# Kernel optimization log

Hardware: AMD Instinct MI355X
Metric: run time of the kernel (lower is better)

## Reference

```python
import jax, jax.numpy as jnp
import numpy as np

B, S, D, H = 2, 2048, 1024, 16
HD = D // H  # head_dim = 64

def setup_inputs() -> dict:
    key = jax.random.key(0)
    ks = jax.random.split(key, 5)
    scale = 0.02
    return {
        "x":  jax.random.normal(ks[0], (B, S, D), dtype=jnp.float32),
        "Wq": jax.random.normal(ks[1], (D, D), dtype=jnp.float32) * scale,
        "Wk": jax.random.normal(ks[2], (D, D), dtype=jnp.float32) * scale,
        "Wv": jax.random.normal(ks[3], (D, D), dtype=jnp.float32) * scale,
        "Wo": jax.random.normal(ks[4], (D, D), dtype=jnp.float32) * scale,
    }

def reference(x, Wq, Wk, Wv, Wo):
    b, s, d = x.shape
    # projections (bias-free linear): [b,s,d] @ [d,d]
    q = (x @ Wq).reshape(b, s, H, HD).transpose(0, 2, 1, 3)  # [b,h,s,hd]
    k = (x @ Wk).reshape(b, s, H, HD).transpose(0, 2, 1, 3)
    v = (x @ Wv).reshape(b, s, H, HD).transpose(0, 2, 1, 3)
    scale = jnp.asarray(1.0 / np.sqrt(HD), dtype=x.dtype)
    scores = jnp.einsum('bhqd,bhkd->bhqk', q, k) * scale  # [b,h,s,s]
    causal = jnp.tril(jnp.ones((s, s), dtype=bool))
    scores = jnp.where(causal, scores, jnp.asarray(-jnp.inf, dtype=scores.dtype))
    attn = jax.nn.softmax(scores, axis=-1)
    out = jnp.einsum('bhqk,bhkd->bhqd', attn, v)  # [b,h,s,hd]
    out = out.transpose(0, 2, 1, 3).reshape(b, s, d)
    return out @ Wo
```

## Files before the change

kernel.cpp:

```cpp
#include <hip/hip_runtime.h>
#include <hip/hip_bf16.h>
#include <cstdint>

typedef __bf16 bf16;
typedef bf16 bf16x8 __attribute__((ext_vector_type(8)));
typedef bf16 bf16x4 __attribute__((ext_vector_type(4)));
typedef float f32x4 __attribute__((ext_vector_type(4)));

#define MFMA16(a, b, c) __builtin_amdgcn_mfma_f32_16x16x32_bf16(a, b, c, 0, 0, 0)

struct rawF { f32x4 a, b; };
__device__ inline rawF ldr(const float* p) {
  rawF r; r.a = *(const f32x4*)p; r.b = *(const f32x4*)(p + 4); return r;
}
__device__ inline bf16x8 ldr(const bf16* p) { return *(const bf16x8*)p; }
__device__ inline bf16x8 cv(const rawF& r) {
  bf16x8 o;
#pragma unroll
  for (int i = 0; i < 4; ++i) { o[i] = (bf16)r.a[i]; o[i + 4] = (bf16)r.b[i]; }
  return o;
}
__device__ inline bf16x8 cv(const bf16x8& r) { return r; }
__device__ inline void stC(bf16* C, size_t i, float v) { C[i] = (bf16)v; }
__device__ inline void stC(float* C, size_t i, float v) { C[i] = v; }

__device__ inline void gl16(const bf16* g, bf16* l) {
  __builtin_amdgcn_global_load_lds(
      (const __attribute__((address_space(1))) void*)g,
      (__attribute__((address_space(3))) void*)l, 16, 0, 0);
}

__device__ inline size_t tile_el(int rowg, int colg) {
  int kq = (colg >> 3) & 3;
  int s = (rowg & 15) ^ kq;
  return ((size_t)(rowg >> 7) * 32 + (colg >> 5)) * 4096 +
         (((rowg >> 6) & 1) << 11) + (((rowg >> 4) & 3) << 9) + (kq << 7) +
         (s << 3) + (colg & 7);
}

__global__ __launch_bounds__(256) void prep_wt(const float* __restrict__ W0,
                                               const float* __restrict__ W1,
                                               const float* __restrict__ W2,
                                               const float* __restrict__ W3,
                                               bf16* __restrict__ Wt, int n) {
  const float* Ws[4] = {W0, W1, W2, W3};
  const float* W = Ws[blockIdx.z];
  bf16* out = Wt + (size_t)blockIdx.z * n * n;
  __shared__ bf16 t[32][33];
  int bx = blockIdx.x * 32, by = blockIdx.y * 32;
  int tx = threadIdx.x & 31, ty = threadIdx.x >> 5;
#pragma unroll
  for (int i = 0; i < 32; i += 8)
    t[ty + i][tx] = (bf16)W[(size_t)(by + ty + i) * n + bx + tx];
  __syncthreads();
#pragma unroll
  for (int i = 0; i < 32; i += 8)
    out[(size_t)(bx + ty + i) * n + by + tx] = t[tx][ty + i];
}

__global__ __launch_bounds__(256) void prep_wt_t(const float* __restrict__ W0,
                                                 const float* __restrict__ W1,
                                                 const float* __restrict__ W2,
                                                 const float* __restrict__ W3,
                                                 bf16* __restrict__ Wt, int n) {
  const float* Ws[4] = {W0, W1, W2, W3};
  const float* W = Ws[blockIdx.z];
  bf16* out = Wt + (size_t)blockIdx.z * n * n;
  __shared__ bf16 t[32][33];
  int bx = blockIdx.x * 32, by = blockIdx.y * 32;
  int tx = threadIdx.x & 31, ty = threadIdx.x >> 5;
#pragma unroll
  for (int i = 0; i < 32; i += 8)
    t[ty + i][tx] = (bf16)W[(size_t)(by + ty + i) * n + bx + tx];
  __syncthreads();
  int tid = threadIdx.x;
  if (tid < 128) {
    int ngl = tid >> 2, kc0 = (tid & 3) * 8;
    bf16x8 o;
#pragma unroll
    for (int j = 0; j < 8; ++j) o[j] = t[kc0 + j][ngl];
    *(bf16x8*)&out[tile_el(bx + ngl, by + kc0)] = o;
  }
}

__global__ __launch_bounds__(256) void vtrans(const bf16* __restrict__ V, bf16* __restrict__ Vt) {
  constexpr int Sn = 2048, Dn = 1024;
  __shared__ bf16 L[64 * 66];
  int s0 = blockIdx.x * 64, bh = blockIdx.y;
  int b = bh >> 4, h = bh & 15;
  int t = threadIdx.x;
  int r = t >> 3, c8 = (t & 7) * 8;
#pragma unroll
  for (int half = 0; half < 2; ++half) {
    int rr = r + half * 32;
    bf16x8 v = *(const bf16x8*)&V[(size_t)(b * Sn + s0 + rr) * Dn + h * 64 + c8];
#pragma unroll
    for (int j = 0; j < 8; ++j) L[(c8 + j) * 66 + rr] = v[j];
  }
  __syncthreads();
  int hd = t >> 3;
#pragma unroll
  for (int half = 0; half < 2; ++half) {
    int hh = hd + half * 32;
    bf16x8 o;
#pragma unroll
    for (int j = 0; j < 8; ++j) o[j] = L[hh * 66 + c8 + j];
    *(bf16x8*)&Vt[(size_t)bh * 64 * Sn + (size_t)hh * Sn + s0 + c8] = o;
  }
}

template <typename TC>
__global__ __launch_bounds__(256) void gemmTh(const float* __restrict__ A,
                                              const bf16* __restrict__ B0,
                                              const bf16* __restrict__ B1,
                                              const bf16* __restrict__ B2,
                                              TC* __restrict__ C0, TC* __restrict__ C1,
                                              TC* __restrict__ C2, int nsteps, int nblk) {
  __shared__ bf16 As[2][4096];
  __shared__ bf16 Bs[2][4096];
  int tid = threadIdx.x, wave = tid >> 6, lane = tid & 63;
  int la = lane & 15, quad = lane >> 4;
  int by = blockIdx.y, sel = by / nblk, nb = by - sel * nblk;
  const bf16* Bt = sel == 0 ? B0 : (sel == 1 ? B1 : B2);
  TC* C = sel == 0 ? C0 : (sel == 1 ? C1 : C2);
  const float* Ab = A + (size_t)blockIdx.x * 128 * 1024;
  const bf16* Btb = Bt + (size_t)nb * nsteps * 4096;
  int so = wave * 512 + lane * 8;

  int ar[2], ac[2], swz[2];
  int sq = tid & 3;
#pragma unroll
  for (int p = 0; p < 2; ++p) {
    int li = (tid + p * 256) * 8;
    ar[p] = li >> 5; ac[p] = li & 31;
    swz[p] = ((ar[p] >> 6) << 12) | (((ar[p] >> 4) & 3) << 10) | (sq << 8) |
             (((ar[p] & 15) ^ sq) << 4);
  }
  int rdA = (wave >> 1) * 2048 + quad * 128 + ((la ^ quad) * 8);
  int rdB = (wave & 1) * 2048 + quad * 128 + ((la ^ quad) * 8);

  f32x4 zero = {0.f, 0.f, 0.f, 0.f};
  f32x4 acc[4][4];
#pragma unroll
  for (int i = 0; i < 4; ++i)
#pragma unroll
    for (int j = 0; j < 4; ++j) acc[i][j] = zero;

  rawF pa[2];
#pragma unroll
  for (int p = 0; p < 2; ++p) pa[p] = ldr(&Ab[(size_t)ar[p] * 1024 + ac[p]]);
  gl16(Btb + so, &Bs[0][so]);
  gl16(Btb + so + 2048, &Bs[0][so + 2048]);

  for (int ks = 0; ks < nsteps; ++ks) {
    int cur = ks & 1;
    *(bf16x8*)((char*)&As[cur][0] + swz[0]) = cv(pa[0]);
    *(bf16x8*)((char*)&As[cur][0] + swz[1]) = cv(pa[1]);
    __syncthreads();
    if (ks + 1 < nsteps) {
      int kc = (ks + 1) * 32;
#pragma unroll
      for (int p = 0; p < 2; ++p) pa[p] = ldr(&Ab[(size_t)ar[p] * 1024 + kc + ac[p]]);
      const bf16* gb = Btb + (size_t)(ks + 1) * 4096;
      gl16(gb + so, &Bs[cur ^ 1][so]);
      gl16(gb + so + 2048, &Bs[cur ^ 1][so + 2048]);
    }
    bf16x8 af[4], bfr[4];
#pragma unroll
    for (int i = 0; i < 4; ++i) af[i] = *(const bf16x8*)&As[cur][rdA + i * 512];
#pragma unroll
    for (int j = 0; j < 4; ++j) bfr[j] = *(const bf16x8*)&Bs[cur][rdB + j * 512];
#pragma unroll
    for (int i = 0; i < 4; ++i)
#pragma unroll
      for (int j = 0; j < 4; ++j) acc[i][j] = MFMA16(af[i], bfr[j], acc[i][j]);
  }
#pragma unroll
  for (int i = 0; i < 4; ++i) {
#pragma unroll
    for (int j = 0; j < 4; ++j) {
      int col = nb * 128 + (wave & 1) * 64 + j * 16 + la;
#pragma unroll
      for (int r = 0; r < 4; ++r) {
        int row = blockIdx.x * 128 + (wave >> 1) * 64 + i * 16 + quad * 4 + r;
        stC(C, (size_t)row * 1024 + col, acc[i][j][r]);
      }
    }
  }
}

template <typename TC>
__global__ __launch_bounds__(256) void gemmT(const bf16* __restrict__ At,
                                             const bf16* __restrict__ B0,
                                             const bf16* __restrict__ B1,
                                             const bf16* __restrict__ B2,
                                             TC* __restrict__ C0, TC* __restrict__ C1,
                                             TC* __restrict__ C2, int nsteps, int nblk) {
  __shared__ bf16 As[2][4096];
  __shared__ bf16 Bs[2][4096];
  int tid = threadIdx.x, wave = tid >> 6, lane = tid & 63;
  int la = lane & 15, quad = lane >> 4;
  int by = blockIdx.y, sel = by / nblk, nb = by - sel * nblk;
  const bf16* Bt = sel == 0 ? B0 : (sel == 1 ? B1 : B2);
  TC* C = sel == 0 ? C0 : (sel == 1 ? C1 : C2);
  const bf16* Atb = At + (size_t)blockIdx.x * nsteps * 4096;
  const bf16* Btb = Bt + (size_t)nb * nsteps * 4096;
  int so = wave * 512 + lane * 8;
  int rdA = (wave >> 1) * 2048 + quad * 128 + ((la ^ quad) * 8);
  int rdB = (wave & 1) * 2048 + quad * 128 + ((la ^ quad) * 8);

  f32x4 zero = {0.f, 0.f, 0.f, 0.f};
  f32x4 acc[4][4];
#pragma unroll
  for (int i = 0; i < 4; ++i)
#pragma unroll
    for (int j = 0; j < 4; ++j) acc[i][j] = zero;

  gl16(Atb + so, &As[0][so]);
  gl16(Atb + so + 2048, &As[0][so + 2048]);
  gl16(Btb + so, &Bs[0][so]);
  gl16(Btb + so + 2048, &Bs[0][so + 2048]);

  int cur = 0;
  for (int ks = 0; ks < nsteps; ++ks) {
    __syncthreads();
    if (ks + 1 < nsteps) {
      const bf16* ga = Atb + (size_t)(ks + 1) * 4096;
      const bf16* gb = Btb + (size_t)(ks + 1) * 4096;
      gl16(ga + so, &As[cur ^ 1][so]);
      gl16(ga + so + 2048, &As[cur ^ 1][so + 2048]);
      gl16(gb + so, &Bs[cur ^ 1][so]);
      gl16(gb + so + 2048, &Bs[cur ^ 1][so + 2048]);
    }
    bf16x8 af[4], bfr[4];
#pragma unroll
    for (int i = 0; i < 4; ++i) af[i] = *(const bf16x8*)&As[cur][rdA + i * 512];
#pragma unroll
    for (int j = 0; j < 4; ++j) bfr[j] = *(const bf16x8*)&Bs[cur][rdB + j * 512];
#pragma unroll
    for (int i = 0; i < 4; ++i)
#pragma unroll
      for (int j = 0; j < 4; ++j) acc[i][j] = MFMA16(af[i], bfr[j], acc[i][j]);
    cur ^= 1;
  }
#pragma unroll
  for (int i = 0; i < 4; ++i) {
#pragma unroll
    for (int j = 0; j < 4; ++j) {
      int col = nb * 128 + (wave & 1) * 64 + j * 16 + la;
#pragma unroll
      for (int r = 0; r < 4; ++r) {
        int row = blockIdx.x * 128 + (wave >> 1) * 64 + i * 16 + quad * 4 + r;
        stC(C, (size_t)row * 1024 + col, acc[i][j][r]);
      }
    }
  }
}

template <typename TA, typename TC, bool BT>
__global__ __launch_bounds__(256) void gemm3(const TA* __restrict__ A,
                                             const void* __restrict__ B0p,
                                             const void* __restrict__ B1p,
                                             const void* __restrict__ B2p,
                                             TC* __restrict__ C0, TC* __restrict__ C1,
                                             TC* __restrict__ C2, int M, int N, int K, int nblk) {
  constexpr int LDA = 40;
  __shared__ bf16 As[BT ? 4096 : 5120];
  __shared__ bf16 Bs[4096];
  int tid = threadIdx.x, wave = tid >> 6, lane = tid & 63;
  int la = lane & 15, quad = lane >> 4;
  int wr = (wave >> 1) * 64, wc = (wave & 1) * 64;
  int by = blockIdx.y;
  int sel = by / nblk;
  int n0 = (by - sel * nblk) * 128;
  const void* Bp = sel == 0 ? B0p : (sel == 1 ? B1p : B2p);
  TC* C = sel == 0 ? C0 : (sel == 1 ? C1 : C2);
  const TA* Ab = A + (size_t)blockIdx.x * 128 * K;
  using TB = typename std::conditional<BT, bf16, float>::type;
  const TB* Bm = (const TB*)Bp;

  int ar[2], ac[2], br[2], bc[2], swz[2];
  int sq = tid & 3;
#pragma unroll
  for (int p = 0; p < 2; ++p) {
    int li = (tid + p * 256) * 8;
    ar[p] = li >> 5; ac[p] = li & 31;
    if (BT) { br[p] = li >> 5; bc[p] = li & 31; }
    else    { br[p] = li >> 7; bc[p] = li & 127; }
    int row = ar[p];
    swz[p] = ((row >> 6) << 12) | (((row >> 4) & 3) << 10) | (sq << 8) |
             ((((row & 15) ^ sq)) << 4);
  }
  int rdA = (wave >> 1) * 4096 + quad * 256 + ((la ^ quad) << 4);
  int rdB = (wave & 1) * 4096 + quad * 256 + ((la ^ quad) << 4);

  f32x4 zero = {0.f, 0.f, 0.f, 0.f};
  f32x4 acc[4][4];
#pragma unroll
  for (int i = 0; i < 4; ++i)
#pragma unroll
    for (int j = 0; j < 4; ++j) acc[i][j] = zero;

  decltype(ldr((const TA*)nullptr)) pa[2];
  decltype(ldr((const TB*)nullptr)) pb[2];
#pragma unroll
  for (int p = 0; p < 2; ++p) {
    pa[p] = ldr(&Ab[(size_t)ar[p] * K + ac[p]]);
    if (BT) pb[p] = ldr(&Bm[(size_t)(n0 + br[p]) * K + bc[p]]);
    else    pb[p] = ldr(&Bm[(size_t)br[p] * N + n0 + bc[p]]);
  }

  for (int k0 = 0; k0 < K; k0 += 32) {
#pragma unroll
    for (int p = 0; p < 2; ++p) {
      if constexpr (BT) {
        *(bf16x8*)((char*)As + swz[p]) = cv(pa[p]);
        *(bf16x8*)((char*)Bs + swz[p]) = cv(pb[p]);
      } else {
        *(bf16x8*)&As[ar[p] * LDA + ac[p]] = cv(pa[p]);
        bf16x8 v = cv(pb[p]);
        int kx = br[p] ^ (((bc[p] >> 3) & 3) << 3);
#pragma unroll
        for (int j = 0; j < 8; ++j) Bs[(bc[p] + j) * 32 + kx] = v[j];
      }
    }
    __syncthreads();
    int k1 = k0 + 32;
    if (k1 < K) {
#pragma unroll
      for (int p = 0; p < 2; ++p) {
        pa[p] = ldr(&Ab[(size_t)ar[p] * K + k1 + ac[p]]);
        if (BT) pb[p] = ldr(&Bm[(size_t)(n0 + br[p]) * K + k1 + bc[p]]);
        else    pb[p] = ldr(&Bm[(size_t)(k1 + br[p]) * N + n0 + bc[p]]);
      }
    }
    bf16x8 af[4], bfr[4];
#pragma unroll
    for (int i = 0; i < 4; ++i) {
      if constexpr (BT)
        af[i] = *(const bf16x8*)((const char*)As + rdA + i * 1024);
      else
        af[i] = *(const bf16x8*)&As[(wr + i * 16 + la) * LDA + quad * 8];
    }
#pragma unroll
    for (int j = 0; j < 4; ++j) {
      if constexpr (BT) {
        bfr[j] = *(const bf16x8*)((const char*)Bs + rdB + j * 1024);
      } else {
        int nr = wc + j * 16 + la;
        bfr[j] = *(const bf16x8*)&Bs[nr * 32 + ((quad * 8) ^ (((nr >> 3) & 3) << 3))];
      }
    }
#pragma unroll
    for (int i = 0; i < 4; ++i)
#pragma unroll
      for (int j = 0; j < 4; ++j) acc[i][j] = MFMA16(af[i], bfr[j], acc[i][j]);
    __syncthreads();
  }
#pragma unroll
  for (int i = 0; i < 4; ++i) {
#pragma unroll
    for (int j = 0; j < 4; ++j) {
      int col = n0 + wc + j * 16 + la;
#pragma unroll
      for (int r = 0; r < 4; ++r) {
        int row = blockIdx.x * 128 + wr + i * 16 + quad * 4 + r;
        stC(C, (size_t)row * N + col, acc[i][j][r]);
      }
    }
  }
}

template <bool OT>
__global__ __launch_bounds__(256) void flash_attn(const bf16* __restrict__ Q,
                                                  const bf16* __restrict__ Kg,
                                                  const bf16* __restrict__ Vtg,
                                                  bf16* __restrict__ O,
                                                  bf16* __restrict__ Ot) {
  constexpr int D = 1024, S = 2048;
  const float MASK = -3.0e4f;
  const float SCL2 = 0.18033688011112042f;
  __shared__ bf16 Ks[2][4096];
  __shared__ bf16 Vs[2][4096];
  __shared__ bf16 Ps[4096];

  int n = blockIdx.x;
  int bh = n & 31;
  int j5 = n >> 5;
  int j = j5 & 15;
  int qt = (j5 & 16) ? j : 31 - j;
  int b = bh >> 4, h = bh & 15;
  int tid = threadIdx.x, wave = tid >> 6, lane = tid & 63;
  int la = lane & 15, quad = lane >> 4;
  const size_t base = (size_t)b * S * D + (size_t)h * 64;
  const bf16* Qg = Q + base;
  const bf16* Kb = Kg + base;
  const bf16* Vb = Vtg + (size_t)bh * 64 * S;
  int r0 = tid >> 3, c0 = (tid & 7) * 8;

  int quads = (tid & 7) & 3, kcs = (tid & 7) >> 2;
  int st0 = (r0 >> 4) * 1024 + kcs * 512 + quads * 128 +
            (((r0 & 15) ^ quads ^ (kcs << 2)) * 8);
  int kvrd0 = quad * 128 + ((la ^ quad) * 8);
  int kvrd1 = 512 + quad * 128 + ((la ^ quad ^ 4) * 8);
  int prd0 = wave * 1024 + quad * 128 + ((la ^ ((quad & 1) << 2)) * 8);
  int prd1 = prd0 + 512;
  int pwb = wave * 1024 + (quad >> 1) * 128 +
            ((la ^ ((quad >> 1) << 2)) * 8) + (quad & 1) * 4;

  f32x4 zero = {0.f, 0.f, 0.f, 0.f};
  int q0 = qt * 64;
  int ntiles = qt + 1;

  bf16x8 aq[2];
  {
    int qrow = q0 + wave * 16 + la;
#pragma unroll
    for (int kc = 0; kc < 2; ++kc) {
      bf16x8 t = *(const bf16x8*)&Qg[(size_t)qrow * D + kc * 32 + quad * 8];
#pragma unroll
      for (int i = 0; i < 8; ++i) t[i] = (bf16)((float)t[i] * SCL2);
      aq[kc] = t;
    }
  }

  f32x4 o[4];
#pragma unroll
  for (int nt = 0; nt < 4; ++nt) o[nt] = zero;
  float m_l = MASK, l_l = 0.f;

  bf16x8 kr0 = *(const bf16x8*)&Kb[(size_t)r0 * D + c0];
  bf16x8 kr1 = *(const bf16x8*)&Kb[(size_t)(r0 + 32) * D + c0];
  bf16x8 vr0 = *(const bf16x8*)&Vb[(size_t)r0 * S + c0];
  bf16x8 vr1 = *(const bf16x8*)&Vb[(size_t)(r0 + 32) * S + c0];

  for (int t = 0; t < ntiles; ++t) {
    int cur = t & 1;
    *(bf16x8*)&Ks[cur][st0] = kr0;
    *(bf16x8*)&Ks[cur][st0 + 2048] = kr1;
    *(bf16x8*)&Vs[cur][st0] = vr0;
    *(bf16x8*)&Vs[cur][st0 + 2048] = vr1;
    __syncthreads();
    if (t + 1 < ntiles) {
      int kb2 = (t + 1) * 64;
      kr0 = *(const bf16x8*)&Kb[(size_t)(kb2 + r0) * D + c0];
      kr1 = *(const bf16x8*)&Kb[(size_t)(kb2 + r0 + 32) * D + c0];
      vr0 = *(const bf16x8*)&Vb[(size_t)r0 * S + kb2 + c0];
      vr1 = *(const bf16x8*)&Vb[(size_t)(r0 + 32) * S + kb2 + c0];
    }

    f32x4 s[4];
    __builtin_amdgcn_s_setprio(1);
#pragma unroll
    for (int nt = 0; nt < 4; ++nt) {
      bf16x8 k0f = *(const bf16x8*)&Ks[cur][nt * 1024 + kvrd0];
      bf16x8 k1f = *(const bf16x8*)&Ks[cur][nt * 1024 + kvrd1];
      f32x4 z = zero;
      z = MFMA16(k0f, aq[0], z);
      z = MFMA16(k1f, aq[1], z);
      s[nt] = z;
    }
    __builtin_amdgcn_s_setprio(0);

    if (t == qt) {
      int qa = q0 + wave * 16 + la;
      int kb = t * 64;
#pragma unroll
      for (int nt = 0; nt < 4; ++nt)
#pragma unroll
        for (int r = 0; r < 4; ++r) {
          int ka = kb + nt * 16 + quad * 4 + r;
          s[nt][r] = (ka > qa) ? MASK : s[nt][r];
        }
    }

    float mx;
    {
      float u0 = fmaxf(fmaxf(s[0][0], s[0][1]), fmaxf(s[0][2], s[0][3]));
      float u1 = fmaxf(fmaxf(s[1][0], s[1][1]), fmaxf(s[1][2], s[1][3]));
      float u2 = fmaxf(fmaxf(s[2][0], s[2][1]), fmaxf(s[2][2], s[2][3]));
      float u3 = fmaxf(fmaxf(s[3][0], s[3][1]), fmaxf(s[3][2], s[3][3]));
      mx = fmaxf(fmaxf(u0, u1), fmaxf(u2, u3));
    }
    mx = fmaxf(mx, m_l);
    mx = fmaxf(mx, __shfl_xor(mx, 16, 64));
    mx = fmaxf(mx, __shfl_xor(mx, 32, 64));

    if (!__all(mx - m_l <= 8.0f)) {
      float alpha = __builtin_amdgcn_exp2f(m_l - mx);
      m_l = mx;
      l_l *= alpha;
      f32x4 abv;
#pragma unroll
      for (int r = 0; r < 4; ++r) abv[r] = __shfl(alpha, quad * 4 + r, 64);
#pragma unroll
      for (int nt = 0; nt < 4; ++nt) o[nt] *= abv;
    }

    f32x4 mlv = {m_l, m_l, m_l, m_l};
    float rs = 0.f;
#pragma unroll
    for (int nt = 0; nt < 4; ++nt) {
      f32x4 d = s[nt] - mlv;
      float p0 = __builtin_amdgcn_exp2f(d[0]);
      float p1 = __builtin_amdgcn_exp2f(d[1]);
      float p2 = __builtin_amdgcn_exp2f(d[2]);
      float p3 = __builtin_amdgcn_exp2f(d[3]);
      s[nt][0] = p0; s[nt][1] = p1; s[nt][2] = p2; s[nt][3] = p3;
      rs += (p0 + p1) + (p2 + p3);
    }
    rs += __shfl_xor(rs, 16, 64);
    rs += __shfl_xor(rs, 32, 64);
    l_l += rs;

#pragma unroll
    for (int nt = 0; nt < 4; ++nt) {
      bf16x4 pk;
#pragma unroll
      for (int r = 0; r < 4; ++r) pk[r] = (bf16)s[nt][r];
      *(bf16x4*)&Ps[pwb + nt * 256] = pk;
    }

    __builtin_amdgcn_s_setprio(1);
    {
      bf16x8 ap0 = *(const bf16x8*)&Ps[prd0];
#pragma unroll
      for (int nt = 0; nt < 4; ++nt) {
        bf16x8 bv = *(const bf16x8*)&Vs[cur][nt * 1024 + kvrd0];
        o[nt] = MFMA16(ap0, bv, o[nt]);
      }
      bf16x8 ap1 = *(const bf16x8*)&Ps[prd1];
#pragma unroll
      for (int nt = 0; nt < 4; ++nt) {
        bf16x8 bv = *(const bf16x8*)&Vs[cur][nt * 1024 + kvrd1];
        o[nt] = MFMA16(ap1, bv, o[nt]);
      }
    }
    __builtin_amdgcn_s_setprio(0);
  }

  f32x4 invv;
#pragma unroll
  for (int r = 0; r < 4; ++r) {
    float lv = __shfl(l_l, quad * 4 + r, 64);
    invv[r] = (lv > 1e-30f) ? 1.0f / lv : 0.0f;
  }
#pragma unroll
  for (int nt = 0; nt < 4; ++nt) {
    o[nt] *= invv;
    int hd = nt * 16 + la;
#pragma unroll
    for (int r = 0; r < 4; ++r) {
      int row = q0 + wave * 16 + quad * 4 + r;
      if (OT) {
        int rowg = b * S + row, colg = h * 64 + hd;
        Ot[tile_el(rowg, colg)] = (bf16)o[nt][r];
      } else {
        O[base + (size_t)row * D + hd] = (bf16)o[nt][r];
      }
    }
  }
}

extern "C" void kernel_launch(void* const* d_in, const int* in_sizes, int n_in,
                              void* d_out, int out_size, void* d_ws, size_t ws_size,
                              hipStream_t stream) {
  constexpr int B = 2, S = 2048, D = 1024;
  constexpr int M = B * S;
  constexpr size_t WN = (size_t)D * D;
  constexpr size_t XN = (size_t)M * D;

  const float* x = (const float*)d_in[0];
  const float* Wq = (const float*)d_in[1];
  const float* Wk = (const float*)d_in[2];
  const float* Wv = (const float*)d_in[3];
  const float* Wo = (const float*)d_in[4];
  float* out = (float*)d_out;

  if (ws_size < 2 * XN * sizeof(bf16)) return;
  bf16* Qb = (bf16*)d_ws;
  bf16* Vtg = Qb + XN;
  bf16* Wt = Vtg + XN;
  bf16* Ot = Wt + 4 * WN;
  bf16* Kb = (bf16*)d_out;
  bf16* Vb = Kb + XN;
  bool use_bt = ws_size >= (2 * XN + 4 * WN) * sizeof(bf16);
  bool big_ws = ws_size >= (3 * XN + 4 * WN) * sizeof(bf16);

  if (big_ws) {
    prep_wt_t<<<dim3(32, 32, 4), 256, 0, stream>>>(Wq, Wk, Wv, Wo, Wt, D);
    gemmTh<bf16><<<dim3(M / 128, 24), 256, 0, stream>>>(x, Wt, Wt + WN, Wt + 2 * WN,
                                                        Qb, Kb, Vb, 32, 8);
    vtrans<<<dim3(S / 64, 32), 256, 0, stream>>>(Vb, Vtg);
    flash_attn<true><<<dim3(1024), 256, 0, stream>>>(Qb, Kb, Vtg, nullptr, Ot);
    gemmT<float><<<dim3(M / 128, 8), 256, 0, stream>>>(Ot, Wt + 3 * WN, Wt + 3 * WN,
                                                       Wt + 3 * WN, out, out, out, 32, 8);
    return;
  }

  dim3 gq(M / 128, 24), gf(M / 128, 8);
  if (use_bt) {
    prep_wt<<<dim3(32, 32, 4), 256, 0, stream>>>(Wq, Wk, Wv, Wo, Wt, D);
    gemm3<float, bf16, true><<<gq, 256, 0, stream>>>(x, Wt, Wt + WN, Wt + 2 * WN,
                                                     Qb, Kb, Vb, M, D, D, 8);
  } else {
    gemm3<float, bf16, false><<<gq, 256, 0, stream>>>(x, Wq, Wk, Wv, Qb, Kb, Vb, M, D, D, 8);
  }
  vtrans<<<dim3(S / 64, 32), 256, 0, stream>>>(Vb, Vtg);
  flash_attn<false><<<dim3(1024), 256, 0, stream>>>(Qb, Kb, Vtg, Qb, nullptr);
  if (use_bt) {
    gemm3<bf16, float, true><<<gf, 256, 0, stream>>>(Qb, Wt + 3 * WN, Wt + 3 * WN, Wt + 3 * WN,
                                                     out, out, out, M, D, D, 8);
  } else {
    gemm3<bf16, float, false><<<gf, 256, 0, stream>>>(Qb, Wo, Wo, Wo, out, out, out, M, D, D, 8);
  }
}
```

Measured before the change: 187.0 us.

## Pre-swizzle K and V into tiled LDS layout for direct global-to-LDS attention loads

After: 190.4 us. No clear change (+1.8%).

```diff
diff --git a/kernel.cpp b/kernel.cpp
--- a/kernel.cpp
+++ b/kernel.cpp
@@ -83,6 +83,7 @@
   }
 }
 
+template <bool TILED>
 __global__ __launch_bounds__(256) void vtrans(const bf16* __restrict__ V, bf16* __restrict__ Vt) {
   constexpr int Sn = 2048, Dn = 1024;
   __shared__ bf16 L[64 * 66];
@@ -105,86 +106,14 @@
     bf16x8 o;
 #pragma unroll
     for (int j = 0; j < 8; ++j) o[j] = L[hh * 66 + c8 + j];
-    *(bf16x8*)&Vt[(size_t)bh * 64 * Sn + (size_t)hh * Sn + s0 + c8] = o;
-  }
-}
-
-template <typename TC>
-__global__ __launch_bounds__(256) void gemmTh(const float* __restrict__ A,
-                                              const bf16* __restrict__ B0,
-                                              const bf16* __restrict__ B1,
-                                              const bf16* __restrict__ B2,
-                                              TC* __restrict__ C0, TC* __restrict__ C1,
-                                              TC* __restrict__ C2, int nsteps, int nblk) {
-  __shared__ bf16 As[2][4096];
-  __shared__ bf16 Bs[2][4096];
-  int tid = threadIdx.x, wave = tid >> 6, lane = tid & 63;
-  int la = lane & 15, quad = lane >> 4;
-  int by = blockIdx.y, sel = by / nblk, nb = by - sel * nblk;
-  const bf16* Bt = sel == 0 ? B0 : (sel == 1 ? B1 : B2);
-  TC* C = sel == 0 ? C0 : (sel == 1 ? C1 : C2);
-  const float* Ab = A + (size_t)blockIdx.x * 128 * 1024;
-  const bf16* Btb = Bt + (size_t)nb * nsteps * 4096;
-  int so = wave * 512 + lane * 8;
-
-  int ar[2], ac[2], swz[2];
-  int sq = tid & 3;
-#pragma unroll
-  for (int p = 0; p < 2; ++p) {
-    int li = (tid + p * 256) * 8;
-    ar[p] = li >> 5; ac[p] = li & 31;
-    swz[p] = ((ar[p] >> 6) << 12) | (((ar[p] >> 4) & 3) << 10) | (sq << 8) |
-             (((ar[p] & 15) ^ sq) << 4);
-  }
-  int rdA = (wave >> 1) * 2048 + quad * 128 + ((la ^ quad) * 8);
-  int rdB = (wave & 1) * 2048 + quad * 128 + ((la ^ quad) * 8);
-
-  f32x4 zero = {0.f, 0.f, 0.f, 0.f};
-  f32x4 acc[4][4];
-#pragma unroll
-  for (int i = 0; i < 4; ++i)
-#pragma unroll
-    for (int j = 0; j < 4; ++j) acc[i][j] = zero;
-
-  rawF pa[2];
-#pragma unroll
-  for (int p = 0; p < 2; ++p) pa[p] = ldr(&Ab[(size_t)ar[p] * 1024 + ac[p]]);
-  gl16(Btb + so, &Bs[0][so]);
-  gl16(Btb + so + 2048, &Bs[0][so + 2048]);
-
-  for (int ks = 0; ks < nsteps; ++ks) {
-    int cur = ks & 1;
-    *(bf16x8*)((char*)&As[cur][0] + swz[0]) = cv(pa[0]);
-    *(bf16x8*)((char*)&As[cur][0] + swz[1]) = cv(pa[1]);
-    __syncthreads();
-    if (ks + 1 < nsteps) {
-      int kc = (ks + 1) * 32;
-#pragma unroll
-      for (int p = 0; p < 2; ++p) pa[p] = ldr(&Ab[(size_t)ar[p] * 1024 + kc + ac[p]]);
-      const bf16* gb = Btb + (size_t)(ks + 1) * 4096;
-      gl16(gb + so, &Bs[cur ^ 1][so]);
-      gl16(gb + so + 2048, &Bs[cur ^ 1][so + 2048]);
-    }
-    bf16x8 af[4], bfr[4];
-#pragma unroll
-    for (int i = 0; i < 4; ++i) af[i] = *(const bf16x8*)&As[cur][rdA + i * 512];
-#pragma unroll
-    for (int j = 0; j < 4; ++j) bfr[j] = *(const bf16x8*)&Bs[cur][rdB + j * 512];
-#pragma unroll
-    for (int i = 0; i < 4; ++i)
-#pragma unroll
-      for (int j = 0; j < 4; ++j) acc[i][j] = MFMA16(af[i], bfr[j], acc[i][j]);
-  }
-#pragma unroll
-  for (int i = 0; i < 4; ++i) {
-#pragma unroll
-    for (int j = 0; j < 4; ++j) {
-      int col = nb * 128 + (wave & 1) * 64 + j * 16 + la;
-#pragma unroll
-      for (int r = 0; r < 4; ++r) {
-        int row = blockIdx.x * 128 + (wave >> 1) * 64 + i * 16 + quad * 4 + r;
-        stC(C, (size_t)row * 1024 + col, acc[i][j][r]);
-      }
+    if (TILED) {
+      int tt = s0 >> 6;
+      int nt = hh >> 4, kc = c8 >> 5, qd = (c8 >> 3) & 3;
+      int sl = (hh & 15) ^ qd ^ (kc << 2);
+      *(bf16x8*)&Vt[(size_t)bh * 131072 + (size_t)tt * 4096 + nt * 1024 + kc * 512 +
+                    qd * 128 + sl * 8] = o;
+    } else {
+      *(bf16x8*)&Vt[(size_t)bh * 64 * Sn + (size_t)hh * Sn + s0 + c8] = o;
     }
   }
 }
@@ -263,7 +192,8 @@
                                              const void* __restrict__ B1p,
                                              const void* __restrict__ B2p,
                                              TC* __restrict__ C0, TC* __restrict__ C1,
-                                             TC* __restrict__ C2, int M, int N, int K, int nblk) {
+                                             TC* __restrict__ C2, int M, int N, int K, int nblk,
+                                             int kswz) {
   constexpr int LDA = 40;
   __shared__ bf16 As[BT ? 4096 : 5120];
   __shared__ bf16 Bs[4096];
@@ -357,6 +287,7 @@
       for (int j = 0; j < 4; ++j) acc[i][j] = MFMA16(af[i], bfr[j], acc[i][j]);
     __syncthreads();
   }
+  bool kfmt = kswz && sel == 1;
 #pragma unroll
   for (int i = 0; i < 4; ++i) {
 #pragma unroll
@@ -365,7 +296,17 @@
 #pragma unroll
       for (int r = 0; r < 4; ++r) {
         int row = blockIdx.x * 128 + wr + i * 16 + quad * 4 + r;
-        stC(C, (size_t)row * N + col, acc[i][j][r]);
+        if (kfmt) {
+          int b_ = row >> 11, s_ = row & 2047;
+          int h_ = col >> 6, hd_ = col & 63;
+          int kc2 = hd_ >> 5, qd = (hd_ >> 3) & 3;
+          int sl = (s_ & 15) ^ qd ^ (kc2 << 2);
+          size_t e = (size_t)(b_ * 16 + h_) * 131072 + (size_t)(s_ >> 6) * 4096 +
+                     (size_t)((s_ >> 4) & 3) * 1024 + kc2 * 512 + qd * 128 + sl * 8 + (hd_ & 7);
+          stC(C, e, acc[i][j][r]);
+        } else {
+          stC(C, (size_t)row * N + col, acc[i][j][r]);
+        }
       }
     }
   }
@@ -373,8 +314,8 @@
 
 template <bool OT>
 __global__ __launch_bounds__(256) void flash_attn(const bf16* __restrict__ Q,
-                                                  const bf16* __restrict__ Kg,
-                                                  const bf16* __restrict__ Vtg,
+                                                  const bf16* __restrict__ Kp,
+                                                  const bf16* __restrict__ Vp,
                                                   bf16* __restrict__ O,
                                                   bf16* __restrict__ Ot) {
   constexpr int D = 1024, S = 2048;
@@ -386,8 +327,190 @@
 
   int n = blockIdx.x;
   int bh = n & 31;
-  int j5 = n >> 5;
-  int j = j5 & 15;
+  int j5 = n >> 5, j = j5 & 15;
+  int qt = (j5 & 16) ? j : 31 - j;
+  int b = bh >> 4, h = bh & 15;
+  int tid = threadIdx.x, wave = tid >> 6, lane = tid & 63;
+  int la = lane & 15, quad = lane >> 4;
+  const size_t base = (size_t)b * S * D + (size_t)h * 64;
+  const bf16* Qg = Q + base;
+  const bf16* Kt = Kp + (size_t)bh * 131072;
+  const bf16* Vt = Vp + (size_t)bh * 131072;
+  int so = tid * 8;
+
+  int kvrd0 = quad * 128 + ((la ^ quad) * 8);
+  int kvrd1 = 512 + quad * 128 + ((la ^ quad ^ 4) * 8);
+  int prd0 = wave * 1024 + quad * 128 + ((la ^ ((quad & 1) << 2)) * 8);
+  int prd1 = prd0 + 512;
+  int pwb = wave * 1024 + (quad >> 1) * 128 +
+            ((la ^ ((quad >> 1) << 2)) * 8) + (quad & 1) * 4;
+
+  f32x4 zero = {0.f, 0.f, 0.f, 0.f};
+  int q0 = qt * 64;
+  int ntiles = qt + 1;
+
+  bf16x8 aq[2];
+  {
+    int qrow = q0 + wave * 16 + la;
+#pragma unroll
+    for (int kc = 0; kc < 2; ++kc) {
+      bf16x8 t = *(const bf16x8*)&Qg[(size_t)qrow * D + kc * 32 + quad * 8];
+#pragma unroll
+      for (int i = 0; i < 8; ++i) t[i] = (bf16)((float)t[i] * SCL2);
+      aq[kc] = t;
+    }
+  }
+
+  f32x4 o[4];
+#pragma unroll
+  for (int nt = 0; nt < 4; ++nt) o[nt] = zero;
+  float m_l = MASK, l_l = 0.f;
+
+  gl16(Kt + so, &Ks[0][so]);
+  gl16(Kt + 2048 + so, &Ks[0][2048 + so]);
+  gl16(Vt + so, &Vs[0][so]);
+  gl16(Vt + 2048 + so, &Vs[0][2048 + so]);
+
+  int cur = 0;
+  for (int t = 0; t < ntiles; ++t) {
+    __syncthreads();
+    if (t + 1 < ntiles) {
+      const bf16* kg = Kt + (size_t)(t + 1) * 4096;
+      const bf16* vg = Vt + (size_t)(t + 1) * 4096;
+      gl16(kg + so, &Ks[cur ^ 1][so]);
+      gl16(kg + 2048 + so, &Ks[cur ^ 1][2048 + so]);
+      gl16(vg + so, &Vs[cur ^ 1][so]);
+      gl16(vg + 2048 + so, &Vs[cur ^ 1][2048 + so]);
+    }
+
+    f32x4 s[4];
+    __builtin_amdgcn_s_setprio(1);
+#pragma unroll
+    for (int nt = 0; nt < 4; ++nt) {
+      bf16x8 k0f = *(const bf16x8*)&Ks[cur][nt * 1024 + kvrd0];
+      bf16x8 k1f = *(const bf16x8*)&Ks[cur][nt * 1024 + kvrd1];
+      f32x4 z = zero;
+      z = MFMA16(k0f, aq[0], z);
+      z = MFMA16(k1f, aq[1], z);
+      s[nt] = z;
+    }
+    __builtin_amdgcn_s_setprio(0);
+
+    if (t == qt) {
+      int qa = q0 + wave * 16 + la;
+      int kb = t * 64;
+#pragma unroll
+      for (int nt = 0; nt < 4; ++nt)
+#pragma unroll
+        for (int r = 0; r < 4; ++r) {
+          int ka = kb + nt * 16 + quad * 4 + r;
+          s[nt][r] = (ka > qa) ? MASK : s[nt][r];
+        }
+    }
+
+    float mx;
+    {
+      float u0 = fmaxf(fmaxf(s[0][0], s[0][1]), fmaxf(s[0][2], s[0][3]));
+      float u1 = fmaxf(fmaxf(s[1][0], s[1][1]), fmaxf(s[1][2], s[1][3]));
+      float u2 = fmaxf(fmaxf(s[2][0], s[2][1]), fmaxf(s[2][2], s[2][3]));
+      float u3 = fmaxf(fmaxf(s[3][0], s[3][1]), fmaxf(s[3][2], s[3][3]));
+      mx = fmaxf(fmaxf(u0, u1), fmaxf(u2, u3));
+    }
+    mx = fmaxf(mx, m_l);
+    mx = fmaxf(mx, __shfl_xor(mx, 16, 64));
+    mx = fmaxf(mx, __shfl_xor(mx, 32, 64));
+
+    if (!__all(mx - m_l <= 8.0f)) {
+      float alpha = __builtin_amdgcn_exp2f(m_l - mx);
+      m_l = mx;
+      l_l *= alpha;
+      f32x4 abv;
+#pragma unroll
+      for (int r = 0; r < 4; ++r) abv[r] = __shfl(alpha, quad * 4 + r, 64);
+#pragma unroll
+      for (int nt = 0; nt < 4; ++nt) o[nt] *= abv;
+    }
+
+    f32x4 mlv = {m_l, m_l, m_l, m_l};
+    float rs = 0.f;
+#pragma unroll
+    for (int nt = 0; nt < 4; ++nt) {
+      f32x4 d = s[nt] - mlv;
+      float p0 = __builtin_amdgcn_exp2f(d[0]);
+      float p1 = __builtin_amdgcn_exp2f(d[1]);
+      float p2 = __builtin_amdgcn_exp2f(d[2]);
+      float p3 = __builtin_amdgcn_exp2f(d[3]);
+      s[nt][0] = p0; s[nt][1] = p1; s[nt][2] = p2; s[nt][3] = p3;
+      rs += (p0 + p1) + (p2 + p3);
+    }
+    rs += __shfl_xor(rs, 16, 64);
+    rs += __shfl_xor(rs, 32, 64);
+    l_l += rs;
+
+#pragma unroll
+    for (int nt = 0; nt < 4; ++nt) {
+      bf16x4 pk;
+#pragma unroll
+      for (int r = 0; r < 4; ++r) pk[r] = (bf16)s[nt][r];
+      *(bf16x4*)&Ps[pwb + nt * 256] = pk;
+    }
+
+    __builtin_amdgcn_s_setprio(1);
+    {
+      bf16x8 ap0 = *(const bf16x8*)&Ps[prd0];
+#pragma unroll
+      for (int nt = 0; nt < 4; ++nt) {
+        bf16x8 bv = *(const bf16x8*)&Vs[cur][nt * 1024 + kvrd0];
+        o[nt] = MFMA16(ap0, bv, o[nt]);
+      }
+      bf16x8 ap1 = *(const bf16x8*)&Ps[prd1];
+#pragma unroll
+      for (int nt = 0; nt < 4; ++nt) {
+        bf16x8 bv = *(const bf16x8*)&Vs[cur][nt * 1024 + kvrd1];
+        o[nt] = MFMA16(ap1, bv, o[nt]);
+      }
+    }
+    __builtin_amdgcn_s_setprio(0);
+    cur ^= 1;
+  }
+
+  f32x4 invv;
+#pragma unroll
+  for (int r = 0; r < 4; ++r) {
+    float lv = __shfl(l_l, quad * 4 + r, 64);
+    invv[r] = (lv > 1e-30f) ? 1.0f / lv : 0.0f;
+  }
+#pragma unroll
+  for (int nt = 0; nt < 4; ++nt) {
+    o[nt] *= invv;
+    int hd = nt * 16 + la;
+#pragma unroll
+    for (int r = 0; r < 4; ++r) {
+      int row = q0 + wave * 16 + quad * 4 + r;
+      if (OT) {
+        int rowg = b * S + row, colg = h * 64 + hd;
+        Ot[tile_el(rowg, colg)] = (bf16)o[nt][r];
+      } else {
+        O[base + (size_t)row * D + hd] = (bf16)o[nt][r];
+      }
+    }
+  }
+}
+
+__global__ __launch_bounds__(256) void flash_rm(const bf16* __restrict__ Q,
+                                                const bf16* __restrict__ Kg,
+                                                const bf16* __restrict__ Vtg,
+                                                bf16* __restrict__ O) {
+  constexpr int D = 1024, S = 2048;
+  const float MASK = -3.0e4f;
+  const float SCL2 = 0.18033688011112042f;
+  __shared__ bf16 Ks[4096];
+  __shared__ bf16 Vs[4096];
+  __shared__ bf16 Ps[4096];
+
+  int n = blockIdx.x;
+  int bh = n & 31;
+  int j5 = n >> 5, j = j5 & 15;
   int qt = (j5 & 16) ? j : 31 - j;
   int b = bh >> 4, h = bh & 15;
   int tid = threadIdx.x, wave = tid >> 6, lane = tid & 63;
@@ -435,11 +558,10 @@
   bf16x8 vr1 = *(const bf16x8*)&Vb[(size_t)(r0 + 32) * S + c0];
 
   for (int t = 0; t < ntiles; ++t) {
-    int cur = t & 1;
-    *(bf16x8*)&Ks[cur][st0] = kr0;
-    *(bf16x8*)&Ks[cur][st0 + 2048] = kr1;
-    *(bf16x8*)&Vs[cur][st0] = vr0;
-    *(bf16x8*)&Vs[cur][st0 + 2048] = vr1;
+    *(bf16x8*)&Ks[st0] = kr0;
+    *(bf16x8*)&Ks[st0 + 2048] = kr1;
+    *(bf16x8*)&Vs[st0] = vr0;
+    *(bf16x8*)&Vs[st0 + 2048] = vr1;
     __syncthreads();
     if (t + 1 < ntiles) {
       int kb2 = (t + 1) * 64;
@@ -450,17 +572,15 @@
     }
 
     f32x4 s[4];
-    __builtin_amdgcn_s_setprio(1);
 #pragma unroll
     for (int nt = 0; nt < 4; ++nt) {
-      bf16x8 k0f = *(const bf16x8*)&Ks[cur][nt * 1024 + kvrd0];
-      bf16x8 k1f = *(const bf16x8*)&Ks[cur][nt * 1024 + kvrd1];
+      bf16x8 k0f = *(const bf16x8*)&Ks[nt * 1024 + kvrd0];
+      bf16x8 k1f = *(const bf16x8*)&Ks[nt * 1024 + kvrd1];
       f32x4 z = zero;
       z = MFMA16(k0f, aq[0], z);
       z = MFMA16(k1f, aq[1], z);
       s[nt] = z;
     }
-    __builtin_amdgcn_s_setprio(0);
 
     if (t == qt) {
       int qa = q0 + wave * 16 + la;
@@ -521,22 +641,21 @@
       *(bf16x4*)&Ps[pwb + nt * 256] = pk;
     }
 
-    __builtin_amdgcn_s_setprio(1);
     {
       bf16x8 ap0 = *(const bf16x8*)&Ps[prd0];
 #pragma unroll
       for (int nt = 0; nt < 4; ++nt) {
-        bf16x8 bv = *(const bf16x8*)&Vs[cur][nt * 1024 + kvrd0];
+        bf16x8 bv = *(const bf16x8*)&Vs[nt * 1024 + kvrd0];
         o[nt] = MFMA16(ap0, bv, o[nt]);
       }
       bf16x8 ap1 = *(const bf16x8*)&Ps[prd1];
 #pragma unroll
       for (int nt = 0; nt < 4; ++nt) {
-        bf16x8 bv = *(const bf16x8*)&Vs[cur][nt * 1024 + kvrd1];
+        bf16x8 bv = *(const bf16x8*)&Vs[nt * 1024 + kvrd1];
         o[nt] = MFMA16(ap1, bv, o[nt]);
       }
     }
-    __builtin_amdgcn_s_setprio(0);
+    __syncthreads();
   }
 
   f32x4 invv;
@@ -552,12 +671,7 @@
 #pragma unroll
     for (int r = 0; r < 4; ++r) {
       int row = q0 + wave * 16 + quad * 4 + r;
-      if (OT) {
-        int rowg = b * S + row, colg = h * 64 + hd;
-        Ot[tile_el(rowg, colg)] = (bf16)o[nt][r];
-      } else {
-        O[base + (size_t)row * D + hd] = (bf16)o[nt][r];
-      }
+      O[base + (size_t)row * D + hd] = (bf16)o[nt][r];
     }
   }
 }
@@ -587,31 +701,32 @@
   bool use_bt = ws_size >= (2 * XN + 4 * WN) * sizeof(bf16);
   bool big_ws = ws_size >= (3 * XN + 4 * WN) * sizeof(bf16);
 
+  dim3 gq(M / 128, 24), gf(M / 128, 8);
   if (big_ws) {
-    prep_wt_t<<<dim3(32, 32, 4), 256, 0, stream>>>(Wq, Wk, Wv, Wo, Wt, D);
-    gemmTh<bf16><<<dim3(M / 128, 24), 256, 0, stream>>>(x, Wt, Wt + WN, Wt + 2 * WN,
-                                                        Qb, Kb, Vb, 32, 8);
-    vtrans<<<dim3(S / 64, 32), 256, 0, stream>>>(Vb, Vtg);
+    prep_wt<<<dim3(32, 32, 3), 256, 0, stream>>>(Wq, Wk, Wv, Wq, Wt, D);
+    prep_wt_t<<<dim3(32, 32, 1), 256, 0, stream>>>(Wo, Wo, Wo, Wo, Wt + 3 * WN, D);
+    gemm3<float, bf16, true><<<gq, 256, 0, stream>>>(x, Wt, Wt + WN, Wt + 2 * WN,
+                                                     Qb, Kb, Vb, M, D, D, 8, 1);
+    vtrans<true><<<dim3(S / 64, 32), 256, 0, stream>>>(Vb, Vtg);
     flash_attn<true><<<dim3(1024), 256, 0, stream>>>(Qb, Kb, Vtg, nullptr, Ot);
-    gemmT<float><<<dim3(M / 128, 8), 256, 0, stream>>>(Ot, Wt + 3 * WN, Wt + 3 * WN,
-                                                       Wt + 3 * WN, out, out, out, 32, 8);
+    gemmT<float><<<gf, 256, 0, stream>>>(Ot, Wt + 3 * WN, Wt + 3 * WN, Wt + 3 * WN,
+                                         out, out, out, 32, 8);
     return;
   }
 
-  dim3 gq(M / 128, 24), gf(M / 128, 8);
   if (use_bt) {
     prep_wt<<<dim3(32, 32, 4), 256, 0, stream>>>(Wq, Wk, Wv, Wo, Wt, D);
     gemm3<float, bf16, true><<<gq, 256, 0, stream>>>(x, Wt, Wt + WN, Wt + 2 * WN,
-                                                     Qb, Kb, Vb, M, D, D, 8);
+                                                     Qb, Kb, Vb, M, D, D, 8, 0);
   } else {
-    gemm3<float, bf16, false><<<gq, 256, 0, stream>>>(x, Wq, Wk, Wv, Qb, Kb, Vb, M, D, D, 8);
-  }
-  vtrans<<<dim3(S / 64, 32), 256, 0, stream>>>(Vb, Vtg);
-  flash_attn<false><<<dim3(1024), 256, 0, stream>>>(Qb, Kb, Vtg, Qb, nullptr);
+    gemm3<float, bf16, false><<<gq, 256, 0, stream>>>(x, Wq, Wk, Wv, Qb, Kb, Vb, M, D, D, 8, 0);
+  }
+  vtrans<false><<<dim3(S / 64, 32), 256, 0, stream>>>(Vb, Vtg);
+  flash_rm<<<dim3(1024), 256, 0, stream>>>(Qb, Kb, Vtg, Qb);
   if (use_bt) {
     gemm3<bf16, float, true><<<gf, 256, 0, stream>>>(Qb, Wt + 3 * WN, Wt + 3 * WN, Wt + 3 * WN,
-                                                     out, out, out, M, D, D, 8);
+                                                     out, out, out, M, D, D, 8, 0);
   } else {
-    gemm3<bf16, float, false><<<gf, 256, 0, stream>>>(Qb, Wo, Wo, Wo, out, out, out, M, D, D, 8);
-  }
-}
+    gemm3<bf16, float, false><<<gf, 256, 0, stream>>>(Qb, Wo, Wo, Wo, out, out, out, M, D, D, 8, 0);
+  }
+}
```
